# Performance work log

Hardware: AMD Instinct MI355X
Metric: run time of the kernel (lower is better)

The kernel has to match this reference:

```python
import jax, jax.numpy as jnp
from jax import lax
import numpy as np

V, H, L, C, T = 32000, 1024, 256, 32, 64
SOS_TOKEN = 0


def _lstm_cell(h, c, x, Wih, Whh, bih, bhh):
    # h,c,x: [1,H]; Wih,Whh: [4H,H] (torch gate order i,f,g,o)
    g = x @ Wih.T + h @ Whh.T + bih + bhh
    i, f, gg, o = jnp.split(g, 4, axis=-1)
    c = jax.nn.sigmoid(f) * c + jax.nn.sigmoid(i) * jnp.tanh(gg)
    h = jax.nn.sigmoid(o) * jnp.tanh(c)
    return h, c


def setup_inputs() -> dict:
    key = jax.random.key(0)
    ks = jax.random.split(key, 24)
    s = 1.0 / np.sqrt(H)
    n = lambda k, shp, sc: (jax.random.normal(k, shp, dtype=jnp.float32) * sc)
    return {
        "word": jax.random.randint(ks[0], (1, T), 0, V),
        "tense": jax.random.randint(ks[1], (1,), 0, 4),
        "use_teacher_forcing": 1,
        "tense_emb": n(ks[2], (4, C), 0.02),
        "enc_emb": n(ks[3], (V, H), 0.02),
        "enc_Wih": n(ks[4], (4 * H, H), s),
        "enc_Whh": n(ks[5], (4 * H, H), s),
        "enc_bih": n(ks[6], (4 * H,), s),
        "enc_bhh": n(ks[7], (4 * H,), s),
        "W_mean": n(ks[8], (L, H), s),
        "b_mean": n(ks[9], (L,), s),
        "W_var": n(ks[10], (L, H), s),
        "b_var": n(ks[11], (L,), s),
        "W_l2h": n(ks[12], (H, L + C), s),
        "b_l2h": n(ks[13], (H,), s),
        "dec_emb": n(ks[14], (V, H), 0.02),
        "dec_Wih": n(ks[15], (4 * H, H), s),
        "dec_Whh": n(ks[16], (4 * H, H), s),
        "dec_bih": n(ks[17], (4 * H,), s),
        "dec_bhh": n(ks[18], (4 * H,), s),
        "W_out": n(ks[19], (V, H), s),
        "b_out": n(ks[20], (V,), s),
        "eps": jax.random.normal(ks[21], (L,), dtype=jnp.float32),
    }


def reference(word, tense, use_teacher_forcing, tense_emb, enc_emb, enc_Wih,
              enc_Whh, enc_bih, enc_bhh, W_mean, b_mean, W_var, b_var,
              W_l2h, b_l2h, dec_emb, dec_Wih, dec_Whh, dec_bih, dec_bhh,
              W_out, b_out, eps):
    tense_e = tense_emb[tense]                       # [1, C]
    # Encoder: initial hidden = [zeros(H-C) | tense_emb]
    h0 = jnp.concatenate([jnp.zeros((1, H - C), tense_e.dtype), tense_e], axis=-1)
    c0 = jnp.zeros((1, H), tense_e.dtype)
    enc_x = enc_emb[word[0]]                         # [T, H]

    def enc_step(carry, x):
        h, c = _lstm_cell(carry[0], carry[1], x[None], enc_Wih, enc_Whh, enc_bih, enc_bhh)
        return (h, c), None

    (h, _c), _ = lax.scan(enc_step, (h0, c0), enc_x)
    mean = h @ W_mean.T + b_mean                     # [1, L]
    logvar = h @ W_var.T + b_var                     # [1, L]
    latent = mean + eps * jnp.exp(0.5 * logvar)      # reparameterize

    dec_h0 = jnp.concatenate([latent, tense_e], axis=-1) @ W_l2h.T + b_l2h  # [1,H]
    dec_c0 = jnp.zeros((1, H), dec_h0.dtype)

    # teacher forcing: inputs are [SOS, word[0][0], ..., word[0][T-2]]
    dec_in = jnp.concatenate([jnp.full((1,), SOS_TOKEN, word.dtype), word[0, :-1]])
    dec_x = jax.nn.relu(dec_emb[dec_in])             # [T, H]

    def dec_step(carry, x):
        h, c = _lstm_cell(carry[0], carry[1], x[None], dec_Wih, dec_Whh, dec_bih, dec_bhh)
        logits = h @ W_out.T + b_out                 # [1, V]
        return (h, c), jax.nn.log_softmax(logits, axis=-1)[0]

    _, pred_distribution = lax.scan(dec_step, (dec_h0, dec_c0), dec_x)  # [T, V]
    pred_output = jnp.argmax(pred_distribution, axis=1)                 # [T]
    return pred_output, pred_distribution, mean, logvar
```

## Files before the change

### kernel.cpp

```cpp
#include <hip/hip_runtime.h>
#include <math.h>

#define Hd 1024
#define Td 64
#define Vd 32000

static const size_t OFF_GENC  = 131072;
static const size_t OFF_GDEC  = 393216;
static const size_t OFF_BSE   = 655360;
static const size_t OFF_BSD   = 659456;
static const size_t OFF_TEN   = 663552;
static const size_t OFF_HALL  = 663584;
static const size_t OFF_STATS = 729120;
static const size_t OFF_MB    = 730144;

#define MB_H_PAIRS  133120u
#define MB_PAIRS    133376u
#define FLAGB       0x3f800000u

__device__ __forceinline__ float fsigm(float x) {
  return __fdividef(1.f, 1.f + __expf(-x));
}
__device__ __forceinline__ float ftanh(float x) {
  return 1.f - __fdividef(2.f, __expf(2.f * x) + 1.f);
}

__device__ __forceinline__ void st_flag(unsigned long long* p, float v) {
  unsigned long long u = 0x3f80000000000000ull | (unsigned long long)__float_as_uint(v);
  __hip_atomic_store(p, u, __ATOMIC_RELAXED, __HIP_MEMORY_SCOPE_AGENT);
}

__device__ __forceinline__ float4 poll16(const float2* p) {
  float4 a;
  for (;;) {
    asm volatile("global_load_dwordx4 %0, %1, off sc0 sc1\n\ts_waitcnt vmcnt(0)"
                 : "=&v"(a) : "v"(p) : "memory");
    if (__float_as_uint(a.y) == FLAGB && __float_as_uint(a.w) == FLAGB) return a;
  }
}

__device__ __forceinline__ void stage1024(const float2* base, float* dst, int tid) {
  float4 a = poll16(base + 2 * tid);
  ((float2*)dst)[tid] = make_float2(a.x, a.z);
  __syncthreads();
}

__global__ void prep_kernel(const int* __restrict__ tense,
                            const float* __restrict__ tense_emb,
                            const float* __restrict__ enc_bih, const float* __restrict__ enc_bhh,
                            const float* __restrict__ dec_bih, const float* __restrict__ dec_bhh,
                            float* __restrict__ ws) {
  int gid = blockIdx.x * blockDim.x + threadIdx.x;
  int gsz = gridDim.x * blockDim.x;
  int tens = tense[0];
  for (int i = gid; i < 4096; i += gsz) {
    ws[OFF_BSE + i] = enc_bih[i] + enc_bhh[i];
    ws[OFF_BSD + i] = dec_bih[i] + dec_bhh[i];
  }
  for (int i = gid; i < 32; i += gsz) ws[OFF_TEN + i] = tense_emb[tens * 32 + i];
  float2* mb = (float2*)(ws + OFF_MB);
  for (int i = gid; i < (int)MB_PAIRS; i += gsz) {
    float2 v;
    if (i < (int)MB_H_PAIRS && (i >> 10) == 0) {
      int j = i & 1023;
      v.x = (j < Hd - 32) ? 0.f : tense_emb[tens * 32 + (j - (Hd - 32))];
      v.y = 1.0f;
    } else { v.x = 0.f; v.y = 0.f; }
    mb[i] = v;
  }
}

__device__ __forceinline__ void gemm_body(const float* __restrict__ W,
                                          const float* __restrict__ x,
                                          const float* __restrict__ bias,
                                          float* __restrict__ out, int R, int rbase) {
  __shared__ float xs[64][68];
  __shared__ float wsh[64][68];
  const int tid = threadIdx.x;
  const int a = tid >> 4;
  const int b = tid & 15;
  const int sr = tid & 63;
  const int kq = (tid >> 6) << 4;
  float acc[4][4];
#pragma unroll
  for (int i = 0; i < 4; ++i)
#pragma unroll
    for (int q = 0; q < 4; ++q) acc[i][q] = 0.f;

  for (int kc = 0; kc < 1024; kc += 64) {
    const float4* gx = (const float4*)(x + (size_t)sr * 1024 + kc + kq);
    const float4* gw = (const float4*)(W + (size_t)(rbase + sr) * 1024 + kc + kq);
    float4 vx0 = gx[0], vx1 = gx[1], vx2 = gx[2], vx3 = gx[3];
    float4 vw0 = gw[0], vw1 = gw[1], vw2 = gw[2], vw3 = gw[3];
    __syncthreads();
    xs[kq +  0][sr] = vx0.x; xs[kq +  1][sr] = vx0.y; xs[kq +  2][sr] = vx0.z; xs[kq +  3][sr] = vx0.w;
    xs[kq +  4][sr] = vx1.x; xs[kq +  5][sr] = vx1.y; xs[kq +  6][sr] = vx1.z; xs[kq +  7][sr] = vx1.w;
    xs[kq +  8][sr] = vx2.x; xs[kq +  9][sr] = vx2.y; xs[kq + 10][sr] = vx2.z; xs[kq + 11][sr] = vx2.w;
    xs[kq + 12][sr] = vx3.x; xs[kq + 13][sr] = vx3.y; xs[kq + 14][sr] = vx3.z; xs[kq + 15][sr] = vx3.w;
    wsh[kq +  0][sr] = vw0.x; wsh[kq +  1][sr] = vw0.y; wsh[kq +  2][sr] = vw0.z; wsh[kq +  3][sr] = vw0.w;
    wsh[kq +  4][sr] = vw1.x; wsh[kq +  5][sr] = vw1.y; wsh[kq +  6][sr] = vw1.z; wsh[kq +  7][sr] = vw1.w;
    wsh[kq +  8][sr] = vw2.x; wsh[kq +  9][sr] = vw2.y; wsh[kq + 10][sr] = vw2.z; wsh[kq + 11][sr] = vw2.w;
    wsh[kq + 12][sr] = vw3.x; wsh[kq + 13][sr] = vw3.y; wsh[kq + 14][sr] = vw3.z; wsh[kq + 15][sr] = vw3.w;
    __syncthreads();
#pragma unroll 8
    for (int kk = 0; kk < 64; ++kk) {
      float4 xv = *(const float4*)&xs[kk][a * 4];
      float4 wv = *(const float4*)&wsh[kk][b * 4];
      acc[0][0] = fmaf(xv.x, wv.x, acc[0][0]); acc[0][1] = fmaf(xv.x, wv.y, acc[0][1]);
      acc[0][2] = fmaf(xv.x, wv.z, acc[0][2]); acc[0][3] = fmaf(xv.x, wv.w, acc[0][3]);
      acc[1][0] = fmaf(xv.y, wv.x, acc[1][0]); acc[1][1] = fmaf(xv.y, wv.y, acc[1][1]);
      acc[1][2] = fmaf(xv.y, wv.z, acc[1][2]); acc[1][3] = fmaf(xv.y, wv.w, acc[1][3]);
      acc[2][0] = fmaf(xv.z, wv.x, acc[2][0]); acc[2][1] = fmaf(xv.z, wv.y, acc[2][1]);
      acc[2][2] = fmaf(xv.z, wv.z, acc[2][2]); acc[2][3] = fmaf(xv.z, wv.w, acc[2][3]);
      acc[3][0] = fmaf(xv.w, wv.x, acc[3][0]); acc[3][1] = fmaf(xv.w, wv.y, acc[3][1]);
      acc[3][2] = fmaf(xv.w, wv.z, acc[3][2]); acc[3][3] = fmaf(xv.w, wv.w, acc[3][3]);
    }
  }
  const int rb = rbase + b * 4;
  float4 bv = *(const float4*)(bias + rb);
#pragma unroll
  for (int i = 0; i < 4; ++i) {
    int t = a * 4 + i;
    float4 o;
    o.x = acc[i][0] + bv.x; o.y = acc[i][1] + bv.y;
    o.z = acc[i][2] + bv.z; o.w = acc[i][3] + bv.w;
    *(float4*)(out + (size_t)t * R + rb) = o;
  }
}

__device__ __forceinline__ void gemm_gather_body(const float* __restrict__ W,
                                                 const float* __restrict__ emb,
                                                 const int* __restrict__ word, int dec_mode,
                                                 const float* __restrict__ bias,
                                                 float* __restrict__ out, int R, int rbase) {
  __shared__ float xs[64][68];
  __shared__ float wsh[64][68];
  const int tid = threadIdx.x;
  const int a = tid >> 4;
  const int b = tid & 15;
  const int sr = tid & 63;
  const int kq = (tid >> 6) << 4;
  const int tok = dec_mode ? ((sr == 0) ? 0 : word[sr - 1]) : word[sr];
  const float* xrow = emb + (size_t)tok * 1024;
  float acc[4][4];
#pragma unroll
  for (int i = 0; i < 4; ++i)
#pragma unroll
    for (int q = 0; q < 4; ++q) acc[i][q] = 0.f;

  for (int kc = 0; kc < 1024; kc += 64) {
    const float4* gx = (const float4*)(xrow + kc + kq);
    const float4* gw = (const float4*)(W + (size_t)(rbase + sr) * 1024 + kc + kq);
    float4 vx0 = gx[0], vx1 = gx[1], vx2 = gx[2], vx3 = gx[3];
    float4 vw0 = gw[0], vw1 = gw[1], vw2 = gw[2], vw3 = gw[3];
    if (dec_mode) {
      vx0.x = fmaxf(vx0.x, 0.f); vx0.y = fmaxf(vx0.y, 0.f); vx0.z = fmaxf(vx0.z, 0.f); vx0.w = fmaxf(vx0.w, 0.f);
      vx1.x = fmaxf(vx1.x, 0.f); vx1.y = fmaxf(vx1.y, 0.f); vx1.z = fmaxf(vx1.z, 0.f); vx1.w = fmaxf(vx1.w, 0.f);
      vx2.x = fmaxf(vx2.x, 0.f); vx2.y = fmaxf(vx2.y, 0.f); vx2.z = fmaxf(vx2.z, 0.f); vx2.w = fmaxf(vx2.w, 0.f);
      vx3.x = fmaxf(vx3.x, 0.f); vx3.y = fmaxf(vx3.y, 0.f); vx3.z = fmaxf(vx3.z, 0.f); vx3.w = fmaxf(vx3.w, 0.f);
    }
    __syncthreads();
    xs[kq +  0][sr] = vx0.x; xs[kq +  1][sr] = vx0.y; xs[kq +  2][sr] = vx0.z; xs[kq +  3][sr] = vx0.w;
    xs[kq +  4][sr] = vx1.x; xs[kq +  5][sr] = vx1.y; xs[kq +  6][sr] = vx1.z; xs[kq +  7][sr] = vx1.w;
    xs[kq +  8][sr] = vx2.x; xs[kq +  9][sr] = vx2.y; xs[kq + 10][sr] = vx2.z; xs[kq + 11][sr] = vx2.w;
    xs[kq + 12][sr] = vx3.x; xs[kq + 13][sr] = vx3.y; xs[kq + 14][sr] = vx3.z; xs[kq + 15][sr] = vx3.w;
    wsh[kq +  0][sr] = vw0.x; wsh[kq +  1][sr] = vw0.y; wsh[kq +  2][sr] = vw0.z; wsh[kq +  3][sr] = vw0.w;
    wsh[kq +  4][sr] = vw1.x; wsh[kq +  5][sr] = vw1.y; wsh[kq +  6][sr] = vw1.z; wsh[kq +  7][sr] = vw1.w;
    wsh[kq +  8][sr] = vw2.x; wsh[kq +  9][sr] = vw2.y; wsh[kq + 10][sr] = vw2.z; wsh[kq + 11][sr] = vw2.w;
    wsh[kq + 12][sr] = vw3.x; wsh[kq + 13][sr] = vw3.y; wsh[kq + 14][sr] = vw3.z; wsh[kq + 15][sr] = vw3.w;
    __syncthreads();
#pragma unroll 8
    for (int kk = 0; kk < 64; ++kk) {
      float4 xv = *(const float4*)&xs[kk][a * 4];
      float4 wv = *(const float4*)&wsh[kk][b * 4];
      acc[0][0] = fmaf(xv.x, wv.x, acc[0][0]); acc[0][1] = fmaf(xv.x, wv.y, acc[0][1]);
      acc[0][2] = fmaf(xv.x, wv.z, acc[0][2]); acc[0][3] = fmaf(xv.x, wv.w, acc[0][3]);
      acc[1][0] = fmaf(xv.y, wv.x, acc[1][0]); acc[1][1] = fmaf(xv.y, wv.y, acc[1][1]);
      acc[1][2] = fmaf(xv.y, wv.z, acc[1][2]); acc[1][3] = fmaf(xv.y, wv.w, acc[1][3]);
      acc[2][0] = fmaf(xv.z, wv.x, acc[2][0]); acc[2][1] = fmaf(xv.z, wv.y, acc[2][1]);
      acc[2][2] = fmaf(xv.z, wv.z, acc[2][2]); acc[2][3] = fmaf(xv.z, wv.w, acc[2][3]);
      acc[3][0] = fmaf(xv.w, wv.x, acc[3][0]); acc[3][1] = fmaf(xv.w, wv.y, acc[3][1]);
      acc[3][2] = fmaf(xv.w, wv.z, acc[3][2]); acc[3][3] = fmaf(xv.w, wv.w, acc[3][3]);
    }
  }
  const int rb = rbase + b * 4;
  float4 bv = *(const float4*)(bias + rb);
#pragma unroll
  for (int i = 0; i < 4; ++i) {
    int t = a * 4 + i;
    float4 o;
    o.x = acc[i][0] + bv.x; o.y = acc[i][1] + bv.y;
    o.z = acc[i][2] + bv.z; o.w = acc[i][3] + bv.w;
    *(float4*)(out + (size_t)t * R + rb) = o;
  }
}

__global__ __launch_bounds__(256, 2) void gemm_kernel(const float* __restrict__ W,
                                                      const float* __restrict__ x,
                                                      const float* __restrict__ bias,
                                                      float* __restrict__ out, int R) {
  gemm_body(W, x, bias, out, R, blockIdx.x * 64);
}

__global__ __launch_bounds__(256, 2) void gemm_dual_kernel(
    const float* __restrict__ enc_emb, const float* __restrict__ dec_emb,
    const int* __restrict__ word,
    const float* __restrict__ W0, const float* __restrict__ b0, float* __restrict__ o0,
    const float* __restrict__ W1, const float* __restrict__ b1, float* __restrict__ o1) {
  if (blockIdx.x < 64)
    gemm_gather_body(W0, enc_emb, word, 0, b0, o0, 4096, blockIdx.x * 64);
  else
    gemm_gather_body(W1, dec_emb, word, 1, b1, o1, 4096, (blockIdx.x - 64) * 64);
}

__device__ __forceinline__ void gload16(const float* base, float* d) {
  asm volatile(
      "global_load_dword %0, %16, off\n\t"
      "global_load_dword %1, %16, off offset:256\n\t"
      "global_load_dword %2, %16, off offset:512\n\t"
      "global_load_dword %3, %16, off offset:768\n\t"
      "global_load_dword %4, %16, off offset:1024\n\t"
      "global_load_dword %5, %16, off offset:1280\n\t"
      "global_load_dword %6, %16, off offset:1536\n\t"
      "global_load_dword %7, %16, off offset:1792\n\t"
      "global_load_dword %8, %16, off offset:2048\n\t"
      "global_load_dword %9, %16, off offset:2304\n\t"
      "global_load_dword %10, %16, off offset:2560\n\t"
      "global_load_dword %11, %16, off offset:2816\n\t"
      "global_load_dword %12, %16, off offset:3072\n\t"
      "global_load_dword %13, %16, off offset:3328\n\t"
      "global_load_dword %14, %16, off offset:3584\n\t"
      "global_load_dword %15, %16, off offset:3840\n\t"
      "s_waitcnt vmcnt(0)"
      : "=&v"(d[0]), "=&v"(d[1]), "=&v"(d[2]), "=&v"(d[3]),
        "=&v"(d[4]), "=&v"(d[5]), "=&v"(d[6]), "=&v"(d[7]),
        "=&v"(d[8]), "=&v"(d[9]), "=&v"(d[10]), "=&v"(d[11]),
        "=&v"(d[12]), "=&v"(d[13]), "=&v"(d[14]), "=&v"(d[15])
      : "v"(base));
}

__global__ __launch_bounds__(512, 2) void seq_kernel(
    const float* __restrict__ enc_Whh, const float* __restrict__ dec_Whh,
    const float* __restrict__ W_mean, const float* __restrict__ b_mean,
    const float* __restrict__ W_var, const float* __restrict__ b_var,
    const float* __restrict__ W_l2h, const float* __restrict__ b_l2h,
    const float* __restrict__ eps, float* __restrict__ ws, float* __restrict__ dout) {
  __shared__ float hsbuf[2][Hd];
  __shared__ float lat[288];
  const int tid = threadIdx.x;
  const int lane = tid & 63;
  const int wid = tid >> 6;
  const int j = blockIdx.x * 8 + wid;

  float2* mb = (float2*)(ws + OFF_MB);
  unsigned long long* mbq = (unsigned long long*)(ws + OFF_MB);
  const float* Genc = ws + OFF_GENC;
  const float* Gdec = ws + OFF_GDEC;
  float* h_all = ws + OFF_HALL;

  float we[4][16], wd[4][16];
#pragma unroll
  for (int r = 0; r < 4; ++r) {
    const size_t ro = (size_t)(r * Hd + j) * Hd + lane;
    gload16(enc_Whh + ro, we[r]);
    gload16(dec_Whh + ro, wd[r]);
  }

  float c_reg = 0.f;
  float gb0 = Genc[j], gb1 = Genc[1024 + j], gb2 = Genc[2048 + j], gb3 = Genc[3072 + j];
  for (int t = 0; t < Td; ++t) {
    stage1024(mb + (size_t)t * 1024, hsbuf[t & 1], tid);
    const float* hs = hsbuf[t & 1];
    float p0 = 0.f, p1 = 0.f, p2 = 0.f, p3 = 0.f;
#pragma unroll
    for (int i = 0; i < 16; ++i) {
      float hv = hs[lane + 64 * i];
      p0 = fmaf(we[0][i], hv, p0);
      p1 = fmaf(we[1][i], hv, p1);
      p2 = fmaf(we[2][i], hv, p2);
      p3 = fmaf(we[3][i], hv, p3);
    }
#pragma unroll
    for (int off = 32; off; off >>= 1) {
      p0 += __shfl_xor(p0, off, 64); p1 += __shfl_xor(p1, off, 64);
      p2 += __shfl_xor(p2, off, 64); p3 += __shfl_xor(p3, off, 64);
    }
    float gi = gb0 + p0, gf = gb1 + p1, gg = gb2 + p2, go = gb3 + p3;
    c_reg = fsigm(gf) * c_reg + fsigm(gi) * ftanh(gg);
    float hval = fsigm(go) * ftanh(c_reg);
    if (lane == 0) st_flag(mbq + (size_t)(t + 1) * 1024 + j, hval);
    if (t + 1 < Td) {
      gb0 = Genc[(t + 1) * 4096 + j];
      gb1 = Genc[(t + 1) * 4096 + 1024 + j];
      gb2 = Genc[(t + 1) * 4096 + 2048 + j];
      gb3 = Genc[(t + 1) * 4096 + 3072 + j];
    }
  }

  if (j < 256) {
    stage1024(mb + (size_t)Td * 1024, hsbuf[0], tid);
    const float* hs = hsbuf[0];
    const float* Wm = W_mean + (size_t)j * Hd;
    const float* Wv = W_var + (size_t)j * Hd;
    float pm = 0.f, pv = 0.f;
#pragma unroll
    for (int i = 0; i < 16; ++i) {
      float hv = hs[lane + 64 * i];
      pm = fmaf(Wm[lane + 64 * i], hv, pm);
      pv = fmaf(Wv[lane + 64 * i], hv, pv);
    }
#pragma unroll
    for (int off = 32; off; off >>= 1) {
      pm += __shfl_xor(pm, off, 64); pv += __shfl_xor(pv, off, 64);
    }
    if (lane == 0) {
      float m = pm + b_mean[j];
      float lv = pv + b_var[j];
      dout[2048064 + j] = m;
      dout[2048320 + j] = lv;
      float latv = m + eps[j] * __expf(0.5f * lv);
      st_flag(mbq + MB_H_PAIRS + j, latv);
    }
  }

  if (tid < 128) {
    float4 a = poll16(mb + MB_H_PAIRS + 2 * tid);
    lat[2 * tid] = a.x; lat[2 * tid + 1] = a.z;
  } else if (tid < 160) {
    lat[256 + (tid - 128)] = ws[OFF_TEN + (tid - 128)];
  }
  __syncthreads();

  {
    const float* Wr = W_l2h + (size_t)j * 288;
    float p = fmaf(Wr[lane], lat[lane], 0.f);
    p = fmaf(Wr[lane + 64], lat[lane + 64], p);
    p = fmaf(Wr[lane + 128], lat[lane + 128], p);
    p = fmaf(Wr[lane + 192], lat[lane + 192], p);
    if (lane < 32) p = fmaf(Wr[lane + 256], lat[lane + 256], p);
#pragma unroll
    for (int off = 32; off; off >>= 1) p += __shfl_xor(p, off, 64);
    if (lane == 0) st_flag(mbq + (size_t)65 * 1024 + j, p + b_l2h[j]);
  }
  __syncthreads();

  c_reg = 0.f;
  gb0 = Gdec[j]; gb1 = Gdec[1024 + j]; gb2 = Gdec[2048 + j]; gb3 = Gdec[3072 + j];
  for (int t = 0; t < Td; ++t) {
    stage1024(mb + (size_t)(65 + t) * 1024, hsbuf[t & 1], tid);
    const float* hs = hsbuf[t & 1];
    float p0 = 0.f, p1 = 0.f, p2 = 0.f, p3 = 0.f;
#pragma unroll
    for (int i = 0; i < 16; ++i) {
      float hv = hs[lane + 64 * i];
      p0 = fmaf(wd[0][i], hv, p0);
      p1 = fmaf(wd[1][i], hv, p1);
      p2 = fmaf(wd[2][i], hv, p2);
      p3 = fmaf(wd[3][i], hv, p3);
    }
#pragma unroll
    for (int off = 32; off; off >>= 1) {
      p0 += __shfl_xor(p0, off, 64); p1 += __shfl_xor(p1, off, 64);
      p2 += __shfl_xor(p2, off, 64); p3 += __shfl_xor(p3, off, 64);
    }
    float gi = gb0 + p0, gf = gb1 + p1, gg = gb2 + p2, go = gb3 + p3;
    c_reg = fsigm(gf) * c_reg + fsigm(gi) * ftanh(gg);
    float hval = fsigm(go) * ftanh(c_reg);
    if (lane == 0) {
      if (t + 1 < Td) st_flag(mbq + (size_t)(66 + t) * 1024 + j, hval);
      h_all[(size_t)t * Hd + j] = hval;
    }
    if (t + 1 < Td) {
      gb0 = Gdec[(t + 1) * 4096 + j];
      gb1 = Gdec[(t + 1) * 4096 + 1024 + j];
      gb2 = Gdec[(t + 1) * 4096 + 2048 + j];
      gb3 = Gdec[(t + 1) * 4096 + 3072 + j];
    }
  }
}

__global__ __launch_bounds__(256) void lstats_kernel(const float* __restrict__ logits,
                                                     float* __restrict__ sd) {
  const int blk = blockIdx.x, t = blk >> 2, q = blk & 3, tid = threadIdx.x;
  const float* row = logits + (size_t)t * Vd + q * 8000;
  __shared__ float sm[256];
  __shared__ int si[256];
  float m = -INFINITY; int mi = 0x7fffffff;
  for (int v = tid; v < 8000; v += 256) {
    float x = row[v];
    if (x > m) { m = x; mi = v; }
  }
  sm[tid] = m; si[tid] = mi;
  __syncthreads();
  for (int s = 128; s > 0; s >>= 1) {
    if (tid < s) {
      float om = sm[tid + s]; int oi = si[tid + s];
      if (om > sm[tid] || (om == sm[tid] && oi < si[tid])) { sm[tid] = om; si[tid] = oi; }
    }
    __syncthreads();
  }
  float rm = sm[0]; int ri = si[0];
  __syncthreads();
  float s = 0.f;
  for (int v = tid; v < 8000; v += 256) s += __expf(row[v] - rm);
  sm[tid] = s;
  __syncthreads();
  for (int st = 128; st > 0; st >>= 1) {
    if (tid < st) sm[tid] += sm[tid + st];
    __syncthreads();
  }
  if (tid == 0) {
    sd[blk * 4 + 0] = rm;
    sd[blk * 4 + 1] = (float)(ri + q * 8000);
    sd[blk * 4 + 2] = sm[0];
  }
}

__global__ __launch_bounds__(256) void lfin_kernel(float* __restrict__ out,
                                                   const float* __restrict__ sd) {
  const int blk = blockIdx.x, t = blk >> 2, q = blk & 3, tid = threadIdx.x;
  float M = -INFINITY;
#pragma unroll
  for (int k = 0; k < 4; ++k) M = fmaxf(M, sd[t * 16 + k * 4]);
  float S = 0.f;
#pragma unroll
  for (int k = 0; k < 4; ++k) S += sd[t * 16 + k * 4 + 2] * __expf(sd[t * 16 + k * 4] - M);
  float corr = M + logf(S);
  float4* r4 = (float4*)(out + 64 + (size_t)t * Vd + q * 8000);
  for (int i = tid; i < 2000; i += 256) {
    float4 v = r4[i];
    v.x -= corr; v.y -= corr; v.z -= corr; v.w -= corr;
    r4[i] = v;
  }
  if (q == 0 && tid == 0) {
    float bm = -INFINITY; int bi = 0;
#pragma unroll
    for (int k = 0; k < 4; ++k) {
      float m = sd[t * 16 + k * 4];
      if (m > bm) { bm = m; bi = (int)sd[t * 16 + k * 4 + 1]; }
    }
    out[t] = (float)bi;
  }
}

extern "C" void kernel_launch(void* const* d_in, const int* in_sizes, int n_in,
                              void* d_out, int out_size, void* d_ws, size_t ws_size,
                              hipStream_t stream) {
  (void)in_sizes; (void)n_in; (void)out_size; (void)ws_size;
  const int* word       = (const int*)d_in[0];
  const int* tense      = (const int*)d_in[1];
  const float* tense_emb = (const float*)d_in[3];
  const float* enc_emb   = (const float*)d_in[4];
  const float* enc_Wih   = (const float*)d_in[5];
  const float* enc_Whh   = (const float*)d_in[6];
  const float* enc_bih   = (const float*)d_in[7];
  const float* enc_bhh   = (const float*)d_in[8];
  const float* W_mean    = (const float*)d_in[9];
  const float* b_mean    = (const float*)d_in[10];
  const float* W_var     = (const float*)d_in[11];
  const float* b_var     = (const float*)d_in[12];
  const float* W_l2h     = (const float*)d_in[13];
  const float* b_l2h     = (const float*)d_in[14];
  const float* dec_emb   = (const float*)d_in[15];
  const float* dec_Wih   = (const float*)d_in[16];
  const float* dec_Whh   = (const float*)d_in[17];
  const float* dec_bih   = (const float*)d_in[18];
  const float* dec_bhh   = (const float*)d_in[19];
  const float* W_out     = (const float*)d_in[20];
  const float* b_out     = (const float*)d_in[21];
  const float* eps       = (const float*)d_in[22];
  float* out = (float*)d_out;
  float* ws  = (float*)d_ws;

  prep_kernel<<<256, 256, 0, stream>>>(tense, tense_emb, enc_bih, enc_bhh,
                                       dec_bih, dec_bhh, ws);
  gemm_dual_kernel<<<128, 256, 0, stream>>>(enc_emb, dec_emb, word,
                                            enc_Wih, ws + OFF_BSE, ws + OFF_GENC,
                                            dec_Wih, ws + OFF_BSD, ws + OFF_GDEC);
  seq_kernel<<<128, 512, 0, stream>>>(enc_Whh, dec_Whh, W_mean, b_mean, W_var, b_var,
                                      W_l2h, b_l2h, eps, ws, out);
  gemm_kernel<<<500, 256, 0, stream>>>(W_out, ws + OFF_HALL, b_out, out + 64, 32000);
  lstats_kernel<<<256, 256, 0, stream>>>(out + 64, ws + OFF_STATS);
  lfin_kernel<<<256, 256, 0, stream>>>(out, ws + OFF_STATS);
}
```

Before: 520.6 us.

## Fuse prep into input GEMM and softmax stats into output GEMM epilogue

Removes the prep kernel by moving the tense/mailbox initialization into the dual input-projection GEMM and summing the two bias vectors in the GEMM epilogue. Drops the separate log-softmax statistics pass by computing per-tile max, argmax and online exp-sum inside the output GEMM epilogue with wave shuffles, writing partials per (timestep, block). The final kernel merges 500 partials per row instead of re-reading the logits. This saves two launches and one full read of the 8 MB logits, at the cost of extra epilogue work and a larger partial-merge step.

```diff
diff --git a/kernel.cpp b/kernel.cpp
--- a/kernel.cpp
+++ b/kernel.cpp
@@ -7,12 +7,10 @@
 
 static const size_t OFF_GENC  = 131072;
 static const size_t OFF_GDEC  = 393216;
-static const size_t OFF_BSE   = 655360;
-static const size_t OFF_BSD   = 659456;
 static const size_t OFF_TEN   = 663552;
 static const size_t OFF_HALL  = 663584;
-static const size_t OFF_STATS = 729120;
 static const size_t OFF_MB    = 730144;
+static const size_t OFF_ST2   = 1000000;
 
 #define MB_H_PAIRS  133120u
 #define MB_PAIRS    133376u
@@ -45,35 +43,12 @@
   __syncthreads();
 }
 
-__global__ void prep_kernel(const int* __restrict__ tense,
-                            const float* __restrict__ tense_emb,
-                            const float* __restrict__ enc_bih, const float* __restrict__ enc_bhh,
-                            const float* __restrict__ dec_bih, const float* __restrict__ dec_bhh,
-                            float* __restrict__ ws) {
-  int gid = blockIdx.x * blockDim.x + threadIdx.x;
-  int gsz = gridDim.x * blockDim.x;
-  int tens = tense[0];
-  for (int i = gid; i < 4096; i += gsz) {
-    ws[OFF_BSE + i] = enc_bih[i] + enc_bhh[i];
-    ws[OFF_BSD + i] = dec_bih[i] + dec_bhh[i];
-  }
-  for (int i = gid; i < 32; i += gsz) ws[OFF_TEN + i] = tense_emb[tens * 32 + i];
-  float2* mb = (float2*)(ws + OFF_MB);
-  for (int i = gid; i < (int)MB_PAIRS; i += gsz) {
-    float2 v;
-    if (i < (int)MB_H_PAIRS && (i >> 10) == 0) {
-      int j = i & 1023;
-      v.x = (j < Hd - 32) ? 0.f : tense_emb[tens * 32 + (j - (Hd - 32))];
-      v.y = 1.0f;
-    } else { v.x = 0.f; v.y = 0.f; }
-    mb[i] = v;
-  }
-}
-
-__device__ __forceinline__ void gemm_body(const float* __restrict__ W,
-                                          const float* __restrict__ x,
-                                          const float* __restrict__ bias,
-                                          float* __restrict__ out, int R, int rbase) {
+__device__ __forceinline__ void gemm_gather_body(const float* __restrict__ W,
+                                                 const float* __restrict__ emb,
+                                                 const int* __restrict__ word, int dec_mode,
+                                                 const float* __restrict__ bih,
+                                                 const float* __restrict__ bhh,
+                                                 float* __restrict__ out, int R, int rbase) {
   __shared__ float xs[64][68];
   __shared__ float wsh[64][68];
   const int tid = threadIdx.x;
@@ -81,6 +56,106 @@
   const int b = tid & 15;
   const int sr = tid & 63;
   const int kq = (tid >> 6) << 4;
+  const int tok = dec_mode ? ((sr == 0) ? 0 : word[sr - 1]) : word[sr];
+  const float* xrow = emb + (size_t)tok * 1024;
+  float acc[4][4];
+#pragma unroll
+  for (int i = 0; i < 4; ++i)
+#pragma unroll
+    for (int q = 0; q < 4; ++q) acc[i][q] = 0.f;
+
+  for (int kc = 0; kc < 1024; kc += 64) {
+    const float4* gx = (const float4*)(xrow + kc + kq);
+    const float4* gw = (const float4*)(W + (size_t)(rbase + sr) * 1024 + kc + kq);
+    float4 vx0 = gx[0], vx1 = gx[1], vx2 = gx[2], vx3 = gx[3];
+    float4 vw0 = gw[0], vw1 = gw[1], vw2 = gw[2], vw3 = gw[3];
+    if (dec_mode) {
+      vx0.x = fmaxf(vx0.x, 0.f); vx0.y = fmaxf(vx0.y, 0.f); vx0.z = fmaxf(vx0.z, 0.f); vx0.w = fmaxf(vx0.w, 0.f);
+      vx1.x = fmaxf(vx1.x, 0.f); vx1.y = fmaxf(vx1.y, 0.f); vx1.z = fmaxf(vx1.z, 0.f); vx1.w = fmaxf(vx1.w, 0.f);
+      vx2.x = fmaxf(vx2.x, 0.f); vx2.y = fmaxf(vx2.y, 0.f); vx2.z = fmaxf(vx2.z, 0.f); vx2.w = fmaxf(vx2.w, 0.f);
+      vx3.x = fmaxf(vx3.x, 0.f); vx3.y = fmaxf(vx3.y, 0.f); vx3.z = fmaxf(vx3.z, 0.f); vx3.w = fmaxf(vx3.w, 0.f);
+    }
+    __syncthreads();
+    xs[kq +  0][sr] = vx0.x; xs[kq +  1][sr] = vx0.y; xs[kq +  2][sr] = vx0.z; xs[kq +  3][sr] = vx0.w;
+    xs[kq +  4][sr] = vx1.x; xs[kq +  5][sr] = vx1.y; xs[kq +  6][sr] = vx1.z; xs[kq +  7][sr] = vx1.w;
+    xs[kq +  8][sr] = vx2.x; xs[kq +  9][sr] = vx2.y; xs[kq + 10][sr] = vx2.z; xs[kq + 11][sr] = vx2.w;
+    xs[kq + 12][sr] = vx3.x; xs[kq + 13][sr] = vx3.y; xs[kq + 14][sr] = vx3.z; xs[kq + 15][sr] = vx3.w;
+    wsh[kq +  0][sr] = vw0.x; wsh[kq +  1][sr] = vw0.y; wsh[kq +  2][sr] = vw0.z; wsh[kq +  3][sr] = vw0.w;
+    wsh[kq +  4][sr] = vw1.x; wsh[kq +  5][sr] = vw1.y; wsh[kq +  6][sr] = vw1.z; wsh[kq +  7][sr] = vw1.w;
+    wsh[kq +  8][sr] = vw2.x; wsh[kq +  9][sr] = vw2.y; wsh[kq + 10][sr] = vw2.z; wsh[kq + 11][sr] = vw2.w;
+    wsh[kq + 12][sr] = vw3.x; wsh[kq + 13][sr] = vw3.y; wsh[kq + 14][sr] = vw3.z; wsh[kq + 15][sr] = vw3.w;
+    __syncthreads();
+#pragma unroll 8
+    for (int kk = 0; kk < 64; ++kk) {
+      float4 xv = *(const float4*)&xs[kk][a * 4];
+      float4 wv = *(const float4*)&wsh[kk][b * 4];
+      acc[0][0] = fmaf(xv.x, wv.x, acc[0][0]); acc[0][1] = fmaf(xv.x, wv.y, acc[0][1]);
+      acc[0][2] = fmaf(xv.x, wv.z, acc[0][2]); acc[0][3] = fmaf(xv.x, wv.w, acc[0][3]);
+      acc[1][0] = fmaf(xv.y, wv.x, acc[1][0]); acc[1][1] = fmaf(xv.y, wv.y, acc[1][1]);
+      acc[1][2] = fmaf(xv.y, wv.z, acc[1][2]); acc[1][3] = fmaf(xv.y, wv.w, acc[1][3]);
+      acc[2][0] = fmaf(xv.z, wv.x, acc[2][0]); acc[2][1] = fmaf(xv.z, wv.y, acc[2][1]);
+      acc[2][2] = fmaf(xv.z, wv.z, acc[2][2]); acc[2][3] = fmaf(xv.z, wv.w, acc[2][3]);
+      acc[3][0] = fmaf(xv.w, wv.x, acc[3][0]); acc[3][1] = fmaf(xv.w, wv.y, acc[3][1]);
+      acc[3][2] = fmaf(xv.w, wv.z, acc[3][2]); acc[3][3] = fmaf(xv.w, wv.w, acc[3][3]);
+    }
+  }
+  const int rb = rbase + b * 4;
+  float4 b1 = *(const float4*)(bih + rb);
+  float4 b2 = *(const float4*)(bhh + rb);
+#pragma unroll
+  for (int i = 0; i < 4; ++i) {
+    int t = a * 4 + i;
+    float4 o;
+    o.x = acc[i][0] + b1.x + b2.x; o.y = acc[i][1] + b1.y + b2.y;
+    o.z = acc[i][2] + b1.z + b2.z; o.w = acc[i][3] + b1.w + b2.w;
+    *(float4*)(out + (size_t)t * R + rb) = o;
+  }
+}
+
+__global__ __launch_bounds__(256, 2) void gemm_dual_kernel(
+    const int* __restrict__ tense, const float* __restrict__ tense_emb,
+    const float* __restrict__ enc_emb, const float* __restrict__ dec_emb,
+    const int* __restrict__ word,
+    const float* __restrict__ W0, const float* __restrict__ bih0,
+    const float* __restrict__ bhh0, float* __restrict__ o0,
+    const float* __restrict__ W1, const float* __restrict__ bih1,
+    const float* __restrict__ bhh1, float* __restrict__ o1,
+    float* __restrict__ ws) {
+  {
+    int gid = blockIdx.x * blockDim.x + threadIdx.x;
+    int gsz = gridDim.x * blockDim.x;
+    int tens = tense[0];
+    if (gid < 32) ws[OFF_TEN + gid] = tense_emb[tens * 32 + gid];
+    float2* mb = (float2*)(ws + OFF_MB);
+    for (int i = gid; i < (int)MB_PAIRS; i += gsz) {
+      float2 v;
+      if (i < (int)MB_H_PAIRS && (i >> 10) == 0) {
+        int j = i & 1023;
+        v.x = (j < Hd - 32) ? 0.f : tense_emb[tens * 32 + (j - (Hd - 32))];
+        v.y = 1.0f;
+      } else { v.x = 0.f; v.y = 0.f; }
+      mb[i] = v;
+    }
+  }
+  if (blockIdx.x < 64)
+    gemm_gather_body(W0, enc_emb, word, 0, bih0, bhh0, o0, 4096, blockIdx.x * 64);
+  else
+    gemm_gather_body(W1, dec_emb, word, 1, bih1, bhh1, o1, 4096, (blockIdx.x - 64) * 64);
+}
+
+__global__ __launch_bounds__(256, 2) void gemm_kernel(const float* __restrict__ W,
+                                                      const float* __restrict__ x,
+                                                      const float* __restrict__ bias,
+                                                      float* __restrict__ out, int R,
+                                                      float* __restrict__ sd) {
+  __shared__ float xs[64][68];
+  __shared__ float wsh[64][68];
+  const int tid = threadIdx.x;
+  const int a = tid >> 4;
+  const int b = tid & 15;
+  const int sr = tid & 63;
+  const int kq = (tid >> 6) << 4;
+  const int rbase = blockIdx.x * 64;
   float acc[4][4];
 #pragma unroll
   for (int i = 0; i < 4; ++i)
@@ -125,92 +200,28 @@
     o.x = acc[i][0] + bv.x; o.y = acc[i][1] + bv.y;
     o.z = acc[i][2] + bv.z; o.w = acc[i][3] + bv.w;
     *(float4*)(out + (size_t)t * R + rb) = o;
-  }
-}
-
-__device__ __forceinline__ void gemm_gather_body(const float* __restrict__ W,
-                                                 const float* __restrict__ emb,
-                                                 const int* __restrict__ word, int dec_mode,
-                                                 const float* __restrict__ bias,
-                                                 float* __restrict__ out, int R, int rbase) {
-  __shared__ float xs[64][68];
-  __shared__ float wsh[64][68];
-  const int tid = threadIdx.x;
-  const int a = tid >> 4;
-  const int b = tid & 15;
-  const int sr = tid & 63;
-  const int kq = (tid >> 6) << 4;
-  const int tok = dec_mode ? ((sr == 0) ? 0 : word[sr - 1]) : word[sr];
-  const float* xrow = emb + (size_t)tok * 1024;
-  float acc[4][4];
-#pragma unroll
-  for (int i = 0; i < 4; ++i)
-#pragma unroll
-    for (int q = 0; q < 4; ++q) acc[i][q] = 0.f;
-
-  for (int kc = 0; kc < 1024; kc += 64) {
-    const float4* gx = (const float4*)(xrow + kc + kq);
-    const float4* gw = (const float4*)(W + (size_t)(rbase + sr) * 1024 + kc + kq);
-    float4 vx0 = gx[0], vx1 = gx[1], vx2 = gx[2], vx3 = gx[3];
-    float4 vw0 = gw[0], vw1 = gw[1], vw2 = gw[2], vw3 = gw[3];
-    if (dec_mode) {
-      vx0.x = fmaxf(vx0.x, 0.f); vx0.y = fmaxf(vx0.y, 0.f); vx0.z = fmaxf(vx0.z, 0.f); vx0.w = fmaxf(vx0.w, 0.f);
-      vx1.x = fmaxf(vx1.x, 0.f); vx1.y = fmaxf(vx1.y, 0.f); vx1.z = fmaxf(vx1.z, 0.f); vx1.w = fmaxf(vx1.w, 0.f);
-      vx2.x = fmaxf(vx2.x, 0.f); vx2.y = fmaxf(vx2.y, 0.f); vx2.z = fmaxf(vx2.z, 0.f); vx2.w = fmaxf(vx2.w, 0.f);
-      vx3.x = fmaxf(vx3.x, 0.f); vx3.y = fmaxf(vx3.y, 0.f); vx3.z = fmaxf(vx3.z, 0.f); vx3.w = fmaxf(vx3.w, 0.f);
-    }
-    __syncthreads();
-    xs[kq +  0][sr] = vx0.x; xs[kq +  1][sr] = vx0.y; xs[kq +  2][sr] = vx0.z; xs[kq +  3][sr] = vx0.w;
-    xs[kq +  4][sr] = vx1.x; xs[kq +  5][sr] = vx1.y; xs[kq +  6][sr] = vx1.z; xs[kq +  7][sr] = vx1.w;
-    xs[kq +  8][sr] = vx2.x; xs[kq +  9][sr] = vx2.y; xs[kq + 10][sr] = vx2.z; xs[kq + 11][sr] = vx2.w;
-    xs[kq + 12][sr] = vx3.x; xs[kq + 13][sr] = vx3.y; xs[kq + 14][sr] = vx3.z; xs[kq + 15][sr] = vx3.w;
-    wsh[kq +  0][sr] = vw0.x; wsh[kq +  1][sr] = vw0.y; wsh[kq +  2][sr] = vw0.z; wsh[kq +  3][sr] = vw0.w;
-    wsh[kq +  4][sr] = vw1.x; wsh[kq +  5][sr] = vw1.y; wsh[kq +  6][sr] = vw1.z; wsh[kq +  7][sr] = vw1.w;
-    wsh[kq +  8][sr] = vw2.x; wsh[kq +  9][sr] = vw2.y; wsh[kq + 10][sr] = vw2.z; wsh[kq + 11][sr] = vw2.w;
-    wsh[kq + 12][sr] = vw3.x; wsh[kq + 13][sr] = vw3.y; wsh[kq + 14][sr] = vw3.z; wsh[kq + 15][sr] = vw3.w;
-    __syncthreads();
-#pragma unroll 8
-    for (int kk = 0; kk < 64; ++kk) {
-      float4 xv = *(const float4*)&xs[kk][a * 4];
-      float4 wv = *(const float4*)&wsh[kk][b * 4];
-      acc[0][0] = fmaf(xv.x, wv.x, acc[0][0]); acc[0][1] = fmaf(xv.x, wv.y, acc[0][1]);
-      acc[0][2] = fmaf(xv.x, wv.z, acc[0][2]); acc[0][3] = fmaf(xv.x, wv.w, acc[0][3]);
-      acc[1][0] = fmaf(xv.y, wv.x, acc[1][0]); acc[1][1] = fmaf(xv.y, wv.y, acc[1][1]);
-      acc[1][2] = fmaf(xv.y, wv.z, acc[1][2]); acc[1][3] = fmaf(xv.y, wv.w, acc[1][3]);
-      acc[2][0] = fmaf(xv.z, wv.x, acc[2][0]); acc[2][1] = fmaf(xv.z, wv.y, acc[2][1]);
-      acc[2][2] = fmaf(xv.z, wv.z, acc[2][2]); acc[2][3] = fmaf(xv.z, wv.w, acc[2][3]);
-      acc[3][0] = fmaf(xv.w, wv.x, acc[3][0]); acc[3][1] = fmaf(xv.w, wv.y, acc[3][1]);
-      acc[3][2] = fmaf(xv.w, wv.z, acc[3][2]); acc[3][3] = fmaf(xv.w, wv.w, acc[3][3]);
-    }
-  }
-  const int rb = rbase + b * 4;
-  float4 bv = *(const float4*)(bias + rb);
-#pragma unroll
-  for (int i = 0; i < 4; ++i) {
-    int t = a * 4 + i;
-    float4 o;
-    o.x = acc[i][0] + bv.x; o.y = acc[i][1] + bv.y;
-    o.z = acc[i][2] + bv.z; o.w = acc[i][3] + bv.w;
-    *(float4*)(out + (size_t)t * R + rb) = o;
-  }
-}
-
-__global__ __launch_bounds__(256, 2) void gemm_kernel(const float* __restrict__ W,
-                                                      const float* __restrict__ x,
-                                                      const float* __restrict__ bias,
-                                                      float* __restrict__ out, int R) {
-  gemm_body(W, x, bias, out, R, blockIdx.x * 64);
-}
-
-__global__ __launch_bounds__(256, 2) void gemm_dual_kernel(
-    const float* __restrict__ enc_emb, const float* __restrict__ dec_emb,
-    const int* __restrict__ word,
-    const float* __restrict__ W0, const float* __restrict__ b0, float* __restrict__ o0,
-    const float* __restrict__ W1, const float* __restrict__ b1, float* __restrict__ o1) {
-  if (blockIdx.x < 64)
-    gemm_gather_body(W0, enc_emb, word, 0, b0, o0, 4096, blockIdx.x * 64);
-  else
-    gemm_gather_body(W1, dec_emb, word, 1, b1, o1, 4096, (blockIdx.x - 64) * 64);
+    float m = o.x; int mi = rb;
+    if (o.y > m) { m = o.y; mi = rb + 1; }
+    if (o.z > m) { m = o.z; mi = rb + 2; }
+    if (o.w > m) { m = o.w; mi = rb + 3; }
+    float s = __expf(o.x - m) + __expf(o.y - m) + __expf(o.z - m) + __expf(o.w - m);
+#pragma unroll
+    for (int off = 1; off < 16; off <<= 1) {
+      float om = __shfl_xor(m, off, 64);
+      int   oi = __shfl_xor(mi, off, 64);
+      float os = __shfl_xor(s, off, 64);
+      if (om > m || (om == m && oi < mi)) {
+        s = os + s * __expf(m - om);
+        m = om; mi = oi;
+      } else {
+        s = s + os * __expf(om - m);
+      }
+    }
+    if (b == 0) {
+      float* p = sd + ((size_t)t * 500 + blockIdx.x) * 4;
+      p[0] = m; p[1] = (float)mi; p[2] = s;
+    }
+  }
 }
 
 __device__ __forceinline__ void gload16(const float* base, float* d) {
@@ -379,68 +390,45 @@
   }
 }
 
-__global__ __launch_bounds__(256) void lstats_kernel(const float* __restrict__ logits,
-                                                     float* __restrict__ sd) {
-  const int blk = blockIdx.x, t = blk >> 2, q = blk & 3, tid = threadIdx.x;
-  const float* row = logits + (size_t)t * Vd + q * 8000;
-  __shared__ float sm[256];
-  __shared__ int si[256];
-  float m = -INFINITY; int mi = 0x7fffffff;
-  for (int v = tid; v < 8000; v += 256) {
-    float x = row[v];
-    if (x > m) { m = x; mi = v; }
-  }
-  sm[tid] = m; si[tid] = mi;
-  __syncthreads();
-  for (int s = 128; s > 0; s >>= 1) {
-    if (tid < s) {
-      float om = sm[tid + s]; int oi = si[tid + s];
-      if (om > sm[tid] || (om == sm[tid] && oi < si[tid])) { sm[tid] = om; si[tid] = oi; }
-    }
-    __syncthreads();
-  }
-  float rm = sm[0]; int ri = si[0];
-  __syncthreads();
-  float s = 0.f;
-  for (int v = tid; v < 8000; v += 256) s += __expf(row[v] - rm);
-  sm[tid] = s;
-  __syncthreads();
-  for (int st = 128; st > 0; st >>= 1) {
-    if (tid < st) sm[tid] += sm[tid + st];
-    __syncthreads();
-  }
-  if (tid == 0) {
-    sd[blk * 4 + 0] = rm;
-    sd[blk * 4 + 1] = (float)(ri + q * 8000);
-    sd[blk * 4 + 2] = sm[0];
-  }
-}
-
 __global__ __launch_bounds__(256) void lfin_kernel(float* __restrict__ out,
                                                    const float* __restrict__ sd) {
   const int blk = blockIdx.x, t = blk >> 2, q = blk & 3, tid = threadIdx.x;
-  float M = -INFINITY;
-#pragma unroll
-  for (int k = 0; k < 4; ++k) M = fmaxf(M, sd[t * 16 + k * 4]);
-  float S = 0.f;
-#pragma unroll
-  for (int k = 0; k < 4; ++k) S += sd[t * 16 + k * 4 + 2] * __expf(sd[t * 16 + k * 4] - M);
-  float corr = M + logf(S);
+  __shared__ float sm[256];
+  __shared__ float ss[256];
+  __shared__ int si[256];
+  float M = -INFINITY, S = 0.f; int MI = 0x7fffffff;
+  for (int k = tid; k < 500; k += 256) {
+    const float* p = sd + ((size_t)t * 500 + k) * 4;
+    float m = p[0]; int mi = (int)p[1]; float s = p[2];
+    if (m > M || (m == M && mi < MI)) {
+      S = s + S * __expf(M - m);
+      M = m; MI = mi;
+    } else {
+      S = S + s * __expf(m - M);
+    }
+  }
+  sm[tid] = M; si[tid] = MI; ss[tid] = S;
+  __syncthreads();
+  for (int st = 128; st > 0; st >>= 1) {
+    if (tid < st) {
+      float om = sm[tid + st]; int oi = si[tid + st]; float os = ss[tid + st];
+      if (om > sm[tid] || (om == sm[tid] && oi < si[tid])) {
+        ss[tid] = os + ss[tid] * __expf(sm[tid] - om);
+        sm[tid] = om; si[tid] = oi;
+      } else {
+        ss[tid] = ss[tid] + os * __expf(om - sm[tid]);
+      }
+    }
+    __syncthreads();
+  }
+  float corr = sm[0] + logf(ss[0]);
   float4* r4 = (float4*)(out + 64 + (size_t)t * Vd + q * 8000);
   for (int i = tid; i < 2000; i += 256) {
     float4 v = r4[i];
     v.x -= corr; v.y -= corr; v.z -= corr; v.w -= corr;
     r4[i] = v;
   }
-  if (q == 0 && tid == 0) {
-    float bm = -INFINITY; int bi = 0;
-#pragma unroll
-    for (int k = 0; k < 4; ++k) {
-      float m = sd[t * 16 + k * 4];
-      if (m > bm) { bm = m; bi = (int)sd[t * 16 + k * 4 + 1]; }
-    }
-    out[t] = (float)bi;
-  }
+  if (q == 0 && tid == 0) out[t] = (float)si[0];
 }
 
 extern "C" void kernel_launch(void* const* d_in, const int* in_sizes, int n_in,
@@ -472,14 +460,12 @@
   float* out = (float*)d_out;
   float* ws  = (float*)d_ws;
 
-  prep_kernel<<<256, 256, 0, stream>>>(tense, tense_emb, enc_bih, enc_bhh,
-                                       dec_bih, dec_bhh, ws);
-  gemm_dual_kernel<<<128, 256, 0, stream>>>(enc_emb, dec_emb, word,
-                                            enc_Wih, ws + OFF_BSE, ws + OFF_GENC,
-                                            dec_Wih, ws + OFF_BSD, ws + OFF_GDEC);
+  gemm_dual_kernel<<<128, 256, 0, stream>>>(tense, tense_emb, enc_emb, dec_emb, word,
+                                            enc_Wih, enc_bih, enc_bhh, ws + OFF_GENC,
+                                            dec_Wih, dec_bih, dec_bhh, ws + OFF_GDEC, ws);
   seq_kernel<<<128, 512, 0, stream>>>(enc_Whh, dec_Whh, W_mean, b_mean, W_var, b_var,
                                       W_l2h, b_l2h, eps, ws, out);
-  gemm_kernel<<<500, 256, 0, stream>>>(W_out, ws + OFF_HALL, b_out, out + 64, 32000);
-  lstats_kernel<<<256, 256, 0, stream>>>(out + 64, ws + OFF_STATS);
-  lfin_kernel<<<256, 256, 0, stream>>>(out, ws + OFF_STATS);
-}
+  gemm_kernel<<<500, 256, 0, stream>>>(W_out, ws + OFF_HALL, b_out, out + 64, 32000,
+                                       ws + OFF_ST2);
+  lfin_kernel<<<256, 256, 0, stream>>>(out, ws + OFF_ST2);
+}
```

Result: faster. 508.6 us (-2.3%).
